# Optimization experiments

Measured on AMD Instinct MI355X. Metric: run time of the kernel, lower is better.

## Reference

```python
import jax, jax.numpy as jnp
import numpy as np


def _l2norm(x, eps=1e-12):
    # F.normalize(dim=-1): x / max(||x||, eps)
    n = jnp.sqrt(jnp.sum(x * x, axis=-1, keepdims=True))
    return x / jnp.maximum(n, eps)


def setup_inputs() -> dict:
    key = jax.random.key(0)
    k1, k2, k3 = jax.random.split(key, 3)
    B, L, D = 4, 8192, 1024
    x = jax.random.normal(k1, (B, L, D), dtype=jnp.float32)
    # RoutingModule initializes q_proj/k_proj to identity; perturb slightly so the
    # projections are exercised but boundary probabilities stay realistic.
    Wq = jnp.eye(D, dtype=jnp.float32) + 0.02 * jax.random.normal(k2, (D, D), jnp.float32)
    Wk = jnp.eye(D, dtype=jnp.float32) + 0.02 * jax.random.normal(k3, (D, D), jnp.float32)
    return {"x": x, "Wq": Wq, "Wk": Wk, "chunk_divisor": 4}


def reference(x, Wq, Wk, chunk_divisor):
    B, L, D = x.shape
    max_chunks = L // chunk_divisor

    # ---- RoutingModule: p_t = 0.5*(1 - cos(q_t, k_{t-1})), p_0 = 1 ----
    q = _l2norm(jnp.einsum('bld,ed->ble', x[:, 1:], Wq))   # [B, L-1, D]
    k = _l2norm(jnp.einsum('bld,ed->ble', x[:, :-1], Wk))  # [B, L-1, D]
    cos_sim = jnp.einsum('bld,bld->bl', q, k)
    p = jnp.clip((1.0 - cos_sim) * 0.5, 0.0, 1.0)
    p = jnp.concatenate([jnp.ones((B, 1), p.dtype), p], axis=1)  # [B, L]
    boundary_mask = p >= 0.5

    # ---- ChunkLayer: gather boundary positions to the front, right-pad ----
    num_chunks = jnp.minimum(jnp.sum(boundary_mask, axis=-1), max_chunks)  # [B]
    token_idx = jnp.arange(L)[None, :] + (~boundary_mask).astype(jnp.int32) * L
    sorted_idx = jnp.argsort(token_idx, axis=1)
    take_idx = sorted_idx[:, :max_chunks]                                   # [B, C]
    chunked = jnp.take_along_axis(x, take_idx[:, :, None], axis=1)          # [B, C, D]
    pad_mask = jnp.arange(max_chunks)[None, :] < num_chunks[:, None]        # [B, C]
    chunked = chunked * pad_mask[:, :, None].astype(chunked.dtype)

    # ---- DeChunkLayer: EMA smoothing via associative scan, then scatter back ----
    C = max_chunks
    p_chunked = jnp.take_along_axis(p, take_idx, axis=1)
    p_chunked = jnp.clip(p_chunked, 1e-4, 1.0 - 1e-4)                       # [B, C]
    decay = jnp.broadcast_to((1.0 - p_chunked)[:, :, None], chunked.shape)  # [B, C, D]
    weighted_x = p_chunked[:, :, None] * chunked
    decay = decay.at[:, 0].set(0.0)
    weighted_x = weighted_x.at[:, 0].set(chunked[:, 0])

    def combine(left, right):
        d_l, v_l = left
        d_r, v_r = right
        return (d_l * d_r, v_r + d_r * v_l)

    _, smoothed = jax.lax.associative_scan(combine, (decay, weighted_x), axis=1)

    chunk_id = jnp.clip(jnp.cumsum(boundary_mask.astype(jnp.int32), axis=1) - 1, 0, C - 1)
    out = jnp.take_along_axis(smoothed, chunk_id[:, :, None], axis=1)       # [B, L, D]
    return out
```

## Files before the change

### kernel.cpp

```cpp
#include <hip/hip_runtime.h>
#include <math.h>

#define B_ 4
#define L_ 8192
#define D_ 1024
#define C_ 2048
#define CG 128
#define NG (C_/CG)
#define TAUF 3.0e-4f
#define MAXF 4096
#define FXF 8

typedef unsigned short ushortt;
using f32x4  = __attribute__((ext_vector_type(4))) float;
using bf16x8 = __attribute__((ext_vector_type(8))) short;

__device__ __forceinline__ ushortt f2bf(float f) {
    unsigned int u = __float_as_uint(f);
    u = (u + 0x7fffu + ((u >> 16) & 1u)) >> 16;
    return (ushortt)u;
}
__device__ __forceinline__ float bf2f(ushortt h) {
    return __uint_as_float(((unsigned int)h) << 16);
}

#define GLOAD16(gsrc, ldst) \
    __builtin_amdgcn_global_load_lds( \
        (const __attribute__((address_space(1))) unsigned int*)(gsrc), \
        (__attribute__((address_space(3))) unsigned int*)(ldst), 16, 0, 0)

__device__ __forceinline__ int swz32(int row, int g) { return g ^ ((row >> 1) & 3); }

__global__ __launch_bounds__(256) void k_prep(
    const float* __restrict__ Wq, const float* __restrict__ Wk,
    ushortt* __restrict__ eqb, ushortt* __restrict__ ekb)
{
    const float* W = blockIdx.y ? Wk : Wq;
    ushortt* E = blockIdx.y ? ekb : eqb;
    size_t i8 = ((size_t)blockIdx.x * 256 + threadIdx.x) * 8;
    int e = (int)(i8 >> 10), k0 = (int)(i8 & 1023);
    float4 a = *(const float4*)&W[i8];
    float4 b = *(const float4*)&W[i8 + 4];
    float v[8] = {a.x, a.y, a.z, a.w, b.x, b.y, b.z, b.w};
    ushortt o[8];
#pragma unroll
    for (int j = 0; j < 8; ++j) {
        float t = v[j] - ((k0 + j == e) ? 1.0f : 0.0f);
        o[j] = f2bf(t);
    }
    *(uint4*)&E[i8] = *(uint4*)o;
}

__global__ __launch_bounds__(256) void k_xb(
    const float* __restrict__ x, ushortt* __restrict__ xb)
{
    size_t i8 = ((size_t)blockIdx.x * 256 + threadIdx.x) * 8;
    float4 a = *(const float4*)&x[i8];
    float4 b = *(const float4*)&x[i8 + 4];
    float v[8] = {a.x, a.y, a.z, a.w, b.x, b.y, b.z, b.w};
    ushortt o[8];
#pragma unroll
    for (int j = 0; j < 8; ++j) o[j] = f2bf(v[j]);
    *(uint4*)&xb[i8] = *(uint4*)o;
}

__global__ __launch_bounds__(512) void k_gemm(
    const ushortt* __restrict__ xb, const ushortt* __restrict__ eqb,
    const ushortt* __restrict__ ekb,
    float* __restrict__ p, int* __restrict__ cnt, int* __restrict__ flags)
{
    __shared__ ushortt xsh[2][129 * 32];
    __shared__ ushortt eqsh[2][256 * 32];
    __shared__ ushortt eksh[2][256 * 32];
    __shared__ float part[128][4][3];

    const int tid = threadIdx.x;
    const int b = blockIdx.y;
    const int t0 = blockIdx.x * 128;
    const int lane = tid & 63;
    const int w = tid >> 6;
    const int wr = w >> 2;
    const int wc = w & 3;
    const int l15 = lane & 15, lg = lane >> 4;

    const int tq = tid & 255;
    const ushortt* egl = (tid < 256) ? eqb : ekb;

    float nq[16], nk[16], dt[16];
#pragma unroll
    for (int i = 0; i < 16; ++i) { nq[i] = 0.f; nk[i] = 0.f; dt[i] = 0.f; }

    f32x4 aqa[4][4], aka[4][4];
#pragma unroll
    for (int rb = 0; rb < 4; ++rb)
#pragma unroll
        for (int cf = 0; cf < 4; ++cf) {
            aqa[rb][cf] = (f32x4){0.f, 0.f, 0.f, 0.f};
            aka[rb][cf] = (f32x4){0.f, 0.f, 0.f, 0.f};
        }

    auto stage = [&](int it, int buf) {
        const int kb = it & 31, nb = it >> 5;
        const int k0 = kb * 32, e0 = nb * 256;
        uint4 extra;
        if (tid < 4)
            extra = *(const uint4*)&xb[((size_t)b * L_ + (t0 + 127)) * D_ + k0 + tid * 8];
        {
            int row = tid >> 2, g = tid & 3;
            int trow = t0 - 1 + row; if (trow < 0) trow = 0;
            const ushortt* src = &xb[((size_t)b * L_ + trow) * D_ + k0 + swz32(row, g) * 8];
            GLOAD16(src, &xsh[buf][tid * 8]);
        }
        ushortt* edst = (tid < 256) ? eqsh[buf] : eksh[buf];
#pragma unroll
        for (int r = 0; r < 4; ++r) {
            int row = r * 64 + (tq >> 2), g = tq & 3;
            const ushortt* src = &egl[(size_t)(e0 + row) * D_ + k0 + swz32(row, g) * 8];
            GLOAD16(src, &edst[r * 2048 + tq * 8]);
        }
        if (tid < 4)
            *(uint4*)&xsh[buf][128 * 32 + tid * 8] = extra;
    };

    stage(0, 0);
    __syncthreads();

    int buf = 0;
    for (int it = 0; it < 128; ++it) {
        if (it + 1 < 128) stage(it + 1, buf ^ 1);
        const ushortt* xsb = xsh[buf];
        const ushortt* eqs = eqsh[buf];
        const ushortt* eks = eksh[buf];
        {
            bf16x8 aq[4], ak[4];
#pragma unroll
            for (int rb = 0; rb < 4; ++rb) {
                int rq = 1 + wr * 64 + rb * 16 + l15;
                int rk = rq - 1;
                aq[rb] = *(const bf16x8*)&xsb[rq * 32 + swz32(rq, lg) * 8];
                ak[rb] = *(const bf16x8*)&xsb[rk * 32 + swz32(rk, lg) * 8];
            }
#pragma unroll
            for (int cf = 0; cf < 4; ++cf) {
                int er = wc * 64 + cf * 16 + l15;
                int off = er * 32 + swz32(er, lg) * 8;
                bf16x8 bq = *(const bf16x8*)&eqs[off];
#pragma unroll
                for (int rb = 0; rb < 4; ++rb)
                    aqa[rb][cf] = __builtin_amdgcn_mfma_f32_16x16x32_bf16(aq[rb], bq, aqa[rb][cf], 0, 0, 0);
                bf16x8 bk = *(const bf16x8*)&eks[off];
#pragma unroll
                for (int rb = 0; rb < 4; ++rb)
                    aka[rb][cf] = __builtin_amdgcn_mfma_f32_16x16x32_bf16(ak[rb], bk, aka[rb][cf], 0, 0, 0);
            }
        }
        if ((it & 31) == 31) {
            const int e0 = (it >> 5) * 256;
#pragma unroll
            for (int rb = 0; rb < 4; ++rb)
#pragma unroll
                for (int cf = 0; cf < 4; ++cf) {
                    const int ecol = e0 + wc * 64 + cf * 16 + l15;
                    const int tb = t0 + wr * 64 + rb * 16 + lg * 4;
                    const ushortt* xc = &xb[((size_t)b * L_ + tb) * D_ + ecol];
                    float xt0 = bf2f(xc[0]), xt1 = bf2f(xc[D_]);
                    float xt2 = bf2f(xc[2 * D_]), xt3 = bf2f(xc[3 * D_]);
                    float xm0 = (tb == 0) ? xt0 : bf2f(xc[-(int)D_]);
                    float xtv[4] = {xt0, xt1, xt2, xt3};
                    float xmv[4] = {xm0, xt0, xt1, xt2};
#pragma unroll
                    for (int r = 0; r < 4; ++r) {
                        float qe = xtv[r] + aqa[rb][cf][r];
                        float ke = xmv[r] + aka[rb][cf][r];
                        const int s = rb * 4 + r;
                        nq[s] = fmaf(qe, qe, nq[s]);
                        nk[s] = fmaf(ke, ke, nk[s]);
                        dt[s] = fmaf(qe, ke, dt[s]);
                    }
                }
#pragma unroll
            for (int rb = 0; rb < 4; ++rb)
#pragma unroll
                for (int cf = 0; cf < 4; ++cf) {
                    aqa[rb][cf] = (f32x4){0.f, 0.f, 0.f, 0.f};
                    aka[rb][cf] = (f32x4){0.f, 0.f, 0.f, 0.f};
                }
        }
        __syncthreads();
        buf ^= 1;
    }

#pragma unroll
    for (int m = 1; m < 16; m <<= 1) {
#pragma unroll
        for (int s = 0; s < 16; ++s) {
            nq[s] += __shfl_xor(nq[s], m);
            nk[s] += __shfl_xor(nk[s], m);
            dt[s] += __shfl_xor(dt[s], m);
        }
    }
    if (l15 == 0) {
#pragma unroll
        for (int s = 0; s < 16; ++s) {
            int rl = wr * 64 + (s >> 2) * 16 + lg * 4 + (s & 3);
            part[rl][wc][0] = nq[s];
            part[rl][wc][1] = nk[s];
            part[rl][wc][2] = dt[s];
        }
    }
    __syncthreads();
    if (tid < 128) {
        int t = t0 + tid;
        float a = part[tid][0][0] + part[tid][1][0] + part[tid][2][0] + part[tid][3][0];
        float c = part[tid][0][1] + part[tid][1][1] + part[tid][2][1] + part[tid][3][1];
        float d = part[tid][0][2] + part[tid][1][2] + part[tid][2][2] + part[tid][3][2];
        float qn = fmaxf(sqrtf(a), 1e-12f);
        float kn = fmaxf(sqrtf(c), 1e-12f);
        float cs = d / (qn * kn);
        float pv = fminf(fmaxf((1.0f - cs) * 0.5f, 0.0f), 1.0f);
        if (t == 0) pv = 1.0f;
        p[b * L_ + t] = pv;
        if (t > 0 && fabsf(cs) < TAUF) {
            int idx = atomicAdd(cnt, 1);
            if (idx < MAXF) flags[idx] = b * L_ + t;
        }
    }
}

__global__ __launch_bounds__(256) void k_fix(
    const float* __restrict__ x, const float* __restrict__ Wq,
    const float* __restrict__ Wk, const int* __restrict__ cnt,
    const int* __restrict__ flags, float* __restrict__ parts)
{
    int n = *cnt; if (n > MAXF) n = MAXF;
    const int m0 = blockIdx.x * FXF;
    if (m0 >= n) return;
    const int e0 = blockIdx.y * 128;

    __shared__ float xs[FXF * 2][1024];
    __shared__ float ws[2][128 * 17];
    __shared__ float comb[FXF * 4][128];
    __shared__ float red2[2][FXF][3];

    const int tid = threadIdx.x;
    const int e = tid & 127;
    const int kh = tid >> 7;

    {
        int row = tid >> 4, c0 = (tid & 15) * 64;
        int f = row >> 1, wh = row & 1;
        int sl = m0 + f;
        int gf = flags[(sl < n) ? sl : m0];
        int fb = gf >> 13, ft = (gf & (L_ - 1)) - wh;
        const float* src = &x[((size_t)fb * L_ + ft) * D_ + c0];
#pragma unroll
        for (int i = 0; i < 16; ++i)
            *(float4*)&xs[row][c0 + i * 4] = *(const float4*)&src[i * 4];
    }

    const int sr = tid >> 1, sk = (tid & 1) * 8;
    const float* gWq = &Wq[(size_t)(e0 + sr) * D_ + sk];
    const float* gWk = &Wk[(size_t)(e0 + sr) * D_ + sk];

    float acc[FXF][2];
#pragma unroll
    for (int f = 0; f < FXF; ++f) { acc[f][0] = 0.f; acc[f][1] = 0.f; }

    float4 pq0 = ((const float4*)gWq)[0], pq1 = ((const float4*)gWq)[1];
    float4 pk0 = ((const float4*)gWk)[0], pk1 = ((const float4*)gWk)[1];

    for (int kc = 0; kc < 64; ++kc) {
        __syncthreads();
        {
            int o = sr * 17 + sk;
            ws[0][o + 0] = pq0.x; ws[0][o + 1] = pq0.y; ws[0][o + 2] = pq0.z; ws[0][o + 3] = pq0.w;
            ws[0][o + 4] = pq1.x; ws[0][o + 5] = pq1.y; ws[0][o + 6] = pq1.z; ws[0][o + 7] = pq1.w;
            ws[1][o + 0] = pk0.x; ws[1][o + 1] = pk0.y; ws[1][o + 2] = pk0.z; ws[1][o + 3] = pk0.w;
            ws[1][o + 4] = pk1.x; ws[1][o + 5] = pk1.y; ws[1][o + 6] = pk1.z; ws[1][o + 7] = pk1.w;
        }
        if (kc + 1 < 64) {
            const float* nq2 = gWq + (kc + 1) * 16;
            const float* nk2 = gWk + (kc + 1) * 16;
            pq0 = ((const float4*)nq2)[0]; pq1 = ((const float4*)nq2)[1];
            pk0 = ((const float4*)nk2)[0]; pk1 = ((const float4*)nk2)[1];
        }
        __syncthreads();
        float wq[8], wk[8];
#pragma unroll
        for (int j = 0; j < 8; ++j) {
            wq[j] = ws[0][e * 17 + kh * 8 + j];
            wk[j] = ws[1][e * 17 + kh * 8 + j];
        }
        const int kbase = kc * 16 + kh * 8;
#pragma unroll
        for (int f = 0; f < FXF; ++f) {
            float aq = acc[f][0], ak = acc[f][1];
#pragma unroll
            for (int j2 = 0; j2 < 2; ++j2) {
                float4 xq = *(const float4*)&xs[f * 2][kbase + j2 * 4];
                float4 xk = *(const float4*)&xs[f * 2 + 1][kbase + j2 * 4];
                aq = fmaf(xq.x, wq[j2 * 4 + 0], aq); aq = fmaf(xq.y, wq[j2 * 4 + 1], aq);
                aq = fmaf(xq.z, wq[j2 * 4 + 2], aq); aq = fmaf(xq.w, wq[j2 * 4 + 3], aq);
                ak = fmaf(xk.x, wk[j2 * 4 + 0], ak); ak = fmaf(xk.y, wk[j2 * 4 + 1], ak);
                ak = fmaf(xk.z, wk[j2 * 4 + 2], ak); ak = fmaf(xk.w, wk[j2 * 4 + 3], ak);
            }
            acc[f][0] = aq; acc[f][1] = ak;
        }
    }

    __syncthreads();
#pragma unroll
    for (int f = 0; f < FXF; ++f) {
        comb[(f * 2 + 0) * 2 + kh][e] = acc[f][0];
        comb[(f * 2 + 1) * 2 + kh][e] = acc[f][1];
    }
    __syncthreads();
    if (tid < 128) {
        float r0[FXF], r1[FXF], r2[FXF];
#pragma unroll
        for (int f = 0; f < FXF; ++f) {
            float q = comb[(f * 2 + 0) * 2 + 0][e] + comb[(f * 2 + 0) * 2 + 1][e];
            float k = comb[(f * 2 + 1) * 2 + 0][e] + comb[(f * 2 + 1) * 2 + 1][e];
            r0[f] = q * q; r1[f] = k * k; r2[f] = q * k;
        }
#pragma unroll
        for (int m = 1; m < 64; m <<= 1) {
#pragma unroll
            for (int f = 0; f < FXF; ++f) {
                r0[f] += __shfl_xor(r0[f], m);
                r1[f] += __shfl_xor(r1[f], m);
                r2[f] += __shfl_xor(r2[f], m);
            }
        }
        if ((tid & 63) == 0) {
            int wv = tid >> 6;
#pragma unroll
            for (int f = 0; f < FXF; ++f) {
                red2[wv][f][0] = r0[f]; red2[wv][f][1] = r1[f]; red2[wv][f][2] = r2[f];
            }
        }
    }
    __syncthreads();
    if (tid < FXF) {
        float A  = red2[0][tid][0] + red2[1][tid][0];
        float Cc = red2[0][tid][1] + red2[1][tid][1];
        float Dd = red2[0][tid][2] + red2[1][tid][2];
        if (m0 + tid < n) {
            size_t o = ((size_t)(m0 + tid) * 8 + blockIdx.y) * 3;
            parts[o] = A; parts[o + 1] = Cc; parts[o + 2] = Dd;
        }
    }
}

__global__ __launch_bounds__(256) void k_fix_final(
    const int* __restrict__ cnt, const int* __restrict__ flags,
    const float* __restrict__ parts, float* __restrict__ p)
{
    int n = *cnt; if (n > MAXF) n = MAXF;
    int f = blockIdx.x * 256 + threadIdx.x;
    if (f >= n) return;
    float a = 0.f, c = 0.f, d = 0.f;
#pragma unroll
    for (int e = 0; e < 8; ++e) {
        size_t o = ((size_t)f * 8 + e) * 3;
        a += parts[o + 0]; c += parts[o + 1]; d += parts[o + 2];
    }
    float qn = fmaxf(sqrtf(a), 1e-12f);
    float kn = fmaxf(sqrtf(c), 1e-12f);
    float cs = d / (qn * kn);
    float pv = fminf(fmaxf((1.0f - cs) * 0.5f, 0.0f), 1.0f);
    p[flags[f]] = pv;
}

__global__ __launch_bounds__(1024) void k_boundaries(
    const float* __restrict__ p, int* __restrict__ take, int* __restrict__ nch,
    float2* __restrict__ cw, int* __restrict__ segev)
{
    const int b = blockIdx.x;
    const int tid = threadIdx.x;
    __shared__ int ssum[1024];
    __shared__ int tl[C_];

    bool m[8];
    int local = 0;
#pragma unroll
    for (int j = 0; j < 8; ++j) {
        int l = tid * 8 + j;
        m[j] = (p[b * L_ + l] >= 0.5f);
        local += m[j] ? 1 : 0;
    }
    ssum[tid] = local;
    __syncthreads();
    for (int off = 1; off < 1024; off <<= 1) {
        int add = (tid >= off) ? ssum[tid - off] : 0;
        __syncthreads();
        ssum[tid] += add;
        __syncthreads();
    }
    const int total = ssum[1023];
    int rank = ssum[tid] - local;
#pragma unroll
    for (int j = 0; j < 8; ++j) {
        if (m[j]) {
            if (rank < C_) { take[b * C_ + rank] = tid * 8 + j; tl[rank] = tid * 8 + j; }
            ++rank;
        }
    }
    const int K = (total < C_) ? total : C_;
    if (tid == 0) nch[b] = K;
    for (int c = total + tid; c < C_; c += 1024) { take[b * C_ + c] = 0; tl[c] = 0; }
    __syncthreads();
    for (int c = tid; c < C_; c += 1024) {
        int idx = tl[c];
        float pc = p[b * L_ + idx];
        pc = fminf(fmaxf(pc, 1e-4f), 1.f - 1e-4f);
        float dc = (c == 0) ? 0.f : (1.f - pc);
        float wv = (c == 0) ? 1.f : pc;
        cw[b * C_ + c] = make_float2(dc, wv);
        segev[b * C_ + c] = (c + 1 < K) ? tl[c + 1] : L_;
    }
}

__global__ __launch_bounds__(256) void k_scan_local(
    const float* __restrict__ x, const int* __restrict__ take,
    const float2* __restrict__ cw, float* __restrict__ E, float* __restrict__ M)
{
    const int g = blockIdx.x, b = blockIdx.y, zq = blockIdx.z;
    const int d = zq * 256 + threadIdx.x;
    const int base = b * C_ + g * CG;

    float s = 0.f, mm = 1.f;
    for (int cc = 0; cc < CG; cc += 4) {
        int4 i4 = *(const int4*)&take[base + cc];
        float2 w0 = cw[base + cc], w1 = cw[base + cc + 1];
        float2 w2 = cw[base + cc + 2], w3 = cw[base + cc + 3];
        float x0 = x[((size_t)b * L_ + i4.x) * D_ + d];
        float x1 = x[((size_t)b * L_ + i4.y) * D_ + d];
        float x2 = x[((size_t)b * L_ + i4.z) * D_ + d];
        float x3 = x[((size_t)b * L_ + i4.w) * D_ + d];
        s = fmaf(w0.x, s, w0.y * x0); mm *= w0.x;
        s = fmaf(w1.x, s, w1.y * x1); mm *= w1.x;
        s = fmaf(w2.x, s, w2.y * x2); mm *= w2.x;
        s = fmaf(w3.x, s, w3.y * x3); mm *= w3.x;
    }
    E[((size_t)b * NG + g) * D_ + d] = s;
    if (threadIdx.x == 0 && zq == 0) M[b * NG + g] = mm;
}

__global__ __launch_bounds__(256) void k_scan_groups(
    const float* __restrict__ E, const float* __restrict__ M, float* __restrict__ carry)
{
    const int gid = blockIdx.x * 256 + threadIdx.x;
    const int b = gid >> 10, d = gid & 1023;
    float s = 0.f;
    for (int g = 0; g < NG; ++g) {
        carry[((size_t)b * NG + g) * D_ + d] = s;
        s = E[((size_t)b * NG + g) * D_ + d] + M[b * NG + g] * s;
    }
}

__global__ __launch_bounds__(256) void k_scan_out(
    const float* __restrict__ x, const int* __restrict__ take,
    const float2* __restrict__ cw, const int* __restrict__ segev,
    const int* __restrict__ nch, const float* __restrict__ carry,
    float* __restrict__ last_s, float* __restrict__ out)
{
    const int g = blockIdx.x, b = blockIdx.y, zq = blockIdx.z;
    const int d = zq * 256 + threadIdx.x;
    const int K = nch[b];
    const int c0 = g * CG;
    if (c0 >= K) return;
    const int c1 = (c0 + CG < K) ? (c0 + CG) : K;
    const int base = b * C_;

    float s = carry[((size_t)b * NG + g) * D_ + d];
    int idx = take[base + c0];
    float2 w0 = cw[base + c0];
    float xv = x[((size_t)b * L_ + idx) * D_ + d];
    for (int c = c0; c < c1; ++c) {
        int idxn = 0; float2 wn = make_float2(0.f, 0.f); float xn = 0.f;
        if (c + 1 < c1) {
            idxn = take[base + c + 1];
            wn = cw[base + c + 1];
            xn = x[((size_t)b * L_ + idxn) * D_ + d];
        }
        s = fmaf(w0.x, s, w0.y * xv);
        if (c == K - 1) {
            last_s[b * D_ + d] = s;
        } else {
            int sege = segev[base + c];
            for (int l = idx; l < sege; ++l)
                out[((size_t)b * L_ + l) * D_ + d] = s;
        }
        idx = idxn; w0 = wn; xv = xn;
    }
}

__global__ __launch_bounds__(256) void k_tail(
    const int* __restrict__ take, const int* __restrict__ nch,
    const float* __restrict__ last_s, float* __restrict__ out)
{
    const int b = blockIdx.y;
    const int tt0 = blockIdx.x * 8;
    const int K = nch[b];
    const int start = take[b * C_ + K - 1];
    if (tt0 + 8 <= start) return;
    float4 v = *(const float4*)&last_s[b * D_ + threadIdx.x * 4];
#pragma unroll
    for (int j = 0; j < 8; ++j) {
        int t = tt0 + j;
        if (t >= start)
            *(float4*)&out[((size_t)b * L_ + t) * D_ + threadIdx.x * 4] = v;
    }
}

extern "C" void kernel_launch(void* const* d_in, const int* in_sizes, int n_in,
                              void* d_out, int out_size, void* d_ws, size_t ws_size,
                              hipStream_t stream)
{
    (void)in_sizes; (void)n_in; (void)out_size;
    const float* x  = (const float*)d_in[0];
    const float* Wq = (const float*)d_in[1];
    const float* Wk = (const float*)d_in[2];
    float* out = (float*)d_out;

    char* ws = (char*)d_ws;
    float*  p      = (float*)(ws + 0);
    int*    take   = (int*)  (ws + 131072);
    int*    nch    = (int*)  (ws + 163840);
    float*  M      = (float*)(ws + 164096);
    float2* cw     = (float2*)(ws + 164608);
    int*    segev  = (int*)  (ws + 230144);
    float*  last_s = (float*)(ws + 262912);
    int*    cnt    = (int*)  (ws + 279296);
    int*    flags  = (int*)  (ws + 279552);
    float*  parts  = (float*)(ws + 295936);
    float*  E      = (float*)(ws + 689152);
    float*  carry  = (float*)(ws + 951296);
    ushortt* eqb   = (ushortt*)(ws + 1213440);
    ushortt* ekb   = (ushortt*)(ws + 3310592);
    if (ws_size < 5407744u) return;

    ushortt* xb = (ushortt*)d_out;

    hipMemsetAsync(cnt, 0, 256, stream);
    k_prep<<<dim3(512, 2), 256, 0, stream>>>(Wq, Wk, eqb, ekb);
    k_xb<<<16384, 256, 0, stream>>>(x, xb);
    k_gemm<<<dim3(64, B_), 512, 0, stream>>>(xb, eqb, ekb, p, cnt, flags);
    k_fix<<<dim3(MAXF / FXF, 8), 256, 0, stream>>>(x, Wq, Wk, cnt, flags, parts);
    k_fix_final<<<MAXF / 256, 256, 0, stream>>>(cnt, flags, parts, p);
    k_boundaries<<<B_, 1024, 0, stream>>>(p, take, nch, cw, segev);
    dim3 g3(NG, B_, 4);
    k_scan_local<<<g3, 256, 0, stream>>>(x, take, cw, E, M);
    k_scan_groups<<<(B_ * D_) / 256, 256, 0, stream>>>(E, M, carry);
    k_scan_out<<<g3, 256, 0, stream>>>(x, take, cw, segev, nch, carry, last_s, out);
    k_tail<<<dim3(L_ / 8, B_), 256, 0, stream>>>(take, nch, last_s, out);
}
```

Before: 442.9 us.

## Split GEMM output columns across two blocks and add separate p finalize kernel

The fused projection GEMM now splits the output dimension in half across a new grid z dimension, so there are twice as many blocks, each with a smaller 128-column tile and fewer accumulators. Launch bounds now request higher occupancy. Per-token partial norms and dot products are written to scratch space inside the output buffer, and a new kernel combines the two halves and computes p and the flag list. The aim is better CU utilisation, since the old grid had only 256 blocks. The cost is that each block re-stages the same x tile, and there is an extra launch plus a global round trip for the partial sums.

```diff
diff --git a/kernel.cpp b/kernel.cpp
--- a/kernel.cpp
+++ b/kernel.cpp
@@ -64,35 +64,35 @@
     *(uint4*)&xb[i8] = *(uint4*)o;
 }
 
-__global__ __launch_bounds__(512) void k_gemm(
+__global__ __launch_bounds__(512, 4) void k_gemm(
     const ushortt* __restrict__ xb, const ushortt* __restrict__ eqb,
-    const ushortt* __restrict__ ekb,
-    float* __restrict__ p, int* __restrict__ cnt, int* __restrict__ flags)
+    const ushortt* __restrict__ ekb, float* __restrict__ partsg)
 {
     __shared__ ushortt xsh[2][129 * 32];
-    __shared__ ushortt eqsh[2][256 * 32];
-    __shared__ ushortt eksh[2][256 * 32];
-    __shared__ float part[128][4][3];
+    __shared__ ushortt eqsh[2][128 * 32];
+    __shared__ ushortt eksh[2][128 * 32];
+    __shared__ float part[128][2][3];
 
     const int tid = threadIdx.x;
     const int b = blockIdx.y;
     const int t0 = blockIdx.x * 128;
+    const int z = blockIdx.z;
     const int lane = tid & 63;
     const int w = tid >> 6;
-    const int wr = w >> 2;
-    const int wc = w & 3;
+    const int wr = w >> 1;
+    const int wc = w & 1;
     const int l15 = lane & 15, lg = lane >> 4;
 
     const int tq = tid & 255;
     const ushortt* egl = (tid < 256) ? eqb : ekb;
 
-    float nq[16], nk[16], dt[16];
-#pragma unroll
-    for (int i = 0; i < 16; ++i) { nq[i] = 0.f; nk[i] = 0.f; dt[i] = 0.f; }
-
-    f32x4 aqa[4][4], aka[4][4];
-#pragma unroll
-    for (int rb = 0; rb < 4; ++rb)
+    float nq[8], nk[8], dt[8];
+#pragma unroll
+    for (int i = 0; i < 8; ++i) { nq[i] = 0.f; nk[i] = 0.f; dt[i] = 0.f; }
+
+    f32x4 aqa[2][4], aka[2][4];
+#pragma unroll
+    for (int rb = 0; rb < 2; ++rb)
 #pragma unroll
         for (int cf = 0; cf < 4; ++cf) {
             aqa[rb][cf] = (f32x4){0.f, 0.f, 0.f, 0.f};
@@ -101,7 +101,7 @@
 
     auto stage = [&](int it, int buf) {
         const int kb = it & 31, nb = it >> 5;
-        const int k0 = kb * 32, e0 = nb * 256;
+        const int k0 = kb * 32, e0 = z * 512 + nb * 128;
         uint4 extra;
         if (tid < 4)
             extra = *(const uint4*)&xb[((size_t)b * L_ + (t0 + 127)) * D_ + k0 + tid * 8];
@@ -113,7 +113,7 @@
         }
         ushortt* edst = (tid < 256) ? eqsh[buf] : eksh[buf];
 #pragma unroll
-        for (int r = 0; r < 4; ++r) {
+        for (int r = 0; r < 2; ++r) {
             int row = r * 64 + (tq >> 2), g = tq & 3;
             const ushortt* src = &egl[(size_t)(e0 + row) * D_ + k0 + swz32(row, g) * 8];
             GLOAD16(src, &edst[r * 2048 + tq * 8]);
@@ -132,10 +132,10 @@
         const ushortt* eqs = eqsh[buf];
         const ushortt* eks = eksh[buf];
         {
-            bf16x8 aq[4], ak[4];
-#pragma unroll
-            for (int rb = 0; rb < 4; ++rb) {
-                int rq = 1 + wr * 64 + rb * 16 + l15;
+            bf16x8 aq[2], ak[2];
+#pragma unroll
+            for (int rb = 0; rb < 2; ++rb) {
+                int rq = 1 + wr * 32 + rb * 16 + l15;
                 int rk = rq - 1;
                 aq[rb] = *(const bf16x8*)&xsb[rq * 32 + swz32(rq, lg) * 8];
                 ak[rb] = *(const bf16x8*)&xsb[rk * 32 + swz32(rk, lg) * 8];
@@ -146,22 +146,22 @@
                 int off = er * 32 + swz32(er, lg) * 8;
                 bf16x8 bq = *(const bf16x8*)&eqs[off];
 #pragma unroll
-                for (int rb = 0; rb < 4; ++rb)
+                for (int rb = 0; rb < 2; ++rb)
                     aqa[rb][cf] = __builtin_amdgcn_mfma_f32_16x16x32_bf16(aq[rb], bq, aqa[rb][cf], 0, 0, 0);
                 bf16x8 bk = *(const bf16x8*)&eks[off];
 #pragma unroll
-                for (int rb = 0; rb < 4; ++rb)
+                for (int rb = 0; rb < 2; ++rb)
                     aka[rb][cf] = __builtin_amdgcn_mfma_f32_16x16x32_bf16(ak[rb], bk, aka[rb][cf], 0, 0, 0);
             }
         }
         if ((it & 31) == 31) {
-            const int e0 = (it >> 5) * 256;
-#pragma unroll
-            for (int rb = 0; rb < 4; ++rb)
+            const int e0 = z * 512 + (it >> 5) * 128;
+#pragma unroll
+            for (int rb = 0; rb < 2; ++rb)
 #pragma unroll
                 for (int cf = 0; cf < 4; ++cf) {
                     const int ecol = e0 + wc * 64 + cf * 16 + l15;
-                    const int tb = t0 + wr * 64 + rb * 16 + lg * 4;
+                    const int tb = t0 + wr * 32 + rb * 16 + lg * 4;
                     const ushortt* xc = &xb[((size_t)b * L_ + tb) * D_ + ecol];
                     float xt0 = bf2f(xc[0]), xt1 = bf2f(xc[D_]);
                     float xt2 = bf2f(xc[2 * D_]), xt3 = bf2f(xc[3 * D_]);
@@ -179,7 +179,7 @@
                     }
                 }
 #pragma unroll
-            for (int rb = 0; rb < 4; ++rb)
+            for (int rb = 0; rb < 2; ++rb)
 #pragma unroll
                 for (int cf = 0; cf < 4; ++cf) {
                     aqa[rb][cf] = (f32x4){0.f, 0.f, 0.f, 0.f};
@@ -193,7 +193,7 @@
 #pragma unroll
     for (int m = 1; m < 16; m <<= 1) {
 #pragma unroll
-        for (int s = 0; s < 16; ++s) {
+        for (int s = 0; s < 8; ++s) {
             nq[s] += __shfl_xor(nq[s], m);
             nk[s] += __shfl_xor(nk[s], m);
             dt[s] += __shfl_xor(dt[s], m);
@@ -201,8 +201,8 @@
     }
     if (l15 == 0) {
 #pragma unroll
-        for (int s = 0; s < 16; ++s) {
-            int rl = wr * 64 + (s >> 2) * 16 + lg * 4 + (s & 3);
+        for (int s = 0; s < 8; ++s) {
+            int rl = wr * 32 + (s >> 2) * 16 + lg * 4 + (s & 3);
             part[rl][wc][0] = nq[s];
             part[rl][wc][1] = nk[s];
             part[rl][wc][2] = dt[s];
@@ -211,19 +211,32 @@
     __syncthreads();
     if (tid < 128) {
         int t = t0 + tid;
-        float a = part[tid][0][0] + part[tid][1][0] + part[tid][2][0] + part[tid][3][0];
-        float c = part[tid][0][1] + part[tid][1][1] + part[tid][2][1] + part[tid][3][1];
-        float d = part[tid][0][2] + part[tid][1][2] + part[tid][2][2] + part[tid][3][2];
-        float qn = fmaxf(sqrtf(a), 1e-12f);
-        float kn = fmaxf(sqrtf(c), 1e-12f);
-        float cs = d / (qn * kn);
-        float pv = fminf(fmaxf((1.0f - cs) * 0.5f, 0.0f), 1.0f);
-        if (t == 0) pv = 1.0f;
-        p[b * L_ + t] = pv;
-        if (t > 0 && fabsf(cs) < TAUF) {
-            int idx = atomicAdd(cnt, 1);
-            if (idx < MAXF) flags[idx] = b * L_ + t;
-        }
+        size_t o = ((size_t)(b * L_ + t) * 2 + z) * 3;
+        partsg[o + 0] = part[tid][0][0] + part[tid][1][0];
+        partsg[o + 1] = part[tid][0][1] + part[tid][1][1];
+        partsg[o + 2] = part[tid][0][2] + part[tid][1][2];
+    }
+}
+
+__global__ __launch_bounds__(256) void k_pfinal(
+    const float* __restrict__ partsg, float* __restrict__ p,
+    int* __restrict__ cnt, int* __restrict__ flags)
+{
+    int gid = blockIdx.x * 256 + threadIdx.x;
+    int t = gid & (L_ - 1);
+    size_t o = (size_t)gid * 6;
+    float a = partsg[o + 0] + partsg[o + 3];
+    float c = partsg[o + 1] + partsg[o + 4];
+    float d = partsg[o + 2] + partsg[o + 5];
+    float qn = fmaxf(sqrtf(a), 1e-12f);
+    float kn = fmaxf(sqrtf(c), 1e-12f);
+    float cs = d / (qn * kn);
+    float pv = fminf(fmaxf((1.0f - cs) * 0.5f, 0.0f), 1.0f);
+    if (t == 0) pv = 1.0f;
+    p[gid] = pv;
+    if (t > 0 && fabsf(cs) < TAUF) {
+        int idx = atomicAdd(cnt, 1);
+        if (idx < MAXF) flags[idx] = gid;
     }
 }
 
@@ -542,11 +555,13 @@
     if (ws_size < 5407744u) return;
 
     ushortt* xb = (ushortt*)d_out;
+    float* partsg = (float*)((char*)d_out + 67108864);
 
     hipMemsetAsync(cnt, 0, 256, stream);
     k_prep<<<dim3(512, 2), 256, 0, stream>>>(Wq, Wk, eqb, ekb);
     k_xb<<<16384, 256, 0, stream>>>(x, xb);
-    k_gemm<<<dim3(64, B_), 512, 0, stream>>>(xb, eqb, ekb, p, cnt, flags);
+    k_gemm<<<dim3(64, B_, 2), 512, 0, stream>>>(xb, eqb, ekb, partsg);
+    k_pfinal<<<(B_ * L_) / 256, 256, 0, stream>>>(partsg, p, cnt, flags);
     k_fix<<<dim3(MAXF / FXF, 8), 256, 0, stream>>>(x, Wq, Wk, cnt, flags, parts);
     k_fix_final<<<MAXF / 256, 256, 0, stream>>>(cnt, flags, parts, p);
     k_boundaries<<<B_, 1024, 0, stream>>>(p, take, nch, cw, segev);
```

After: 408.6 us. 7.8% less time.
